# Performance work log

Hardware: AMD Instinct MI355X
Metric: run time of the kernel (lower is better)

The kernel has to match this reference:

```python
import jax, jax.numpy as jnp
import numpy as np

H = 16  # num_attention_heads


def setup_inputs() -> dict:
    key = jax.random.key(0)
    ks = jax.random.split(key, 4)
    B, S, D = 2, 2048, 1024
    hidden_states = jax.random.normal(ks[0], (B, S, D), dtype=jnp.float32)
    attention_mask = jnp.zeros((B, 1, 1, S), dtype=jnp.float32)
    scale = 1.0 / np.sqrt(D)
    Wq = jax.random.normal(ks[1], (D, D), dtype=jnp.float32) * scale
    Wk = jax.random.normal(ks[2], (D, D), dtype=jnp.float32) * scale
    Wv = jax.random.normal(ks[3], (D, D), dtype=jnp.float32) * scale
    bq = jnp.zeros((D,), dtype=jnp.float32)
    bk = jnp.zeros((D,), dtype=jnp.float32)
    bv = jnp.zeros((D,), dtype=jnp.float32)
    return {"hidden_states": hidden_states, "attention_mask": attention_mask,
            "Wq": Wq, "bq": bq, "Wk": Wk, "bk": bk, "Wv": Wv, "bv": bv}


def reference(hidden_states, attention_mask, Wq, bq, Wk, bk, Wv, bv):
    B, S, D = hidden_states.shape
    Dh = D // H

    def proj(W, b):
        # torch Linear: x @ W.T + b ; reshape to [B, H, S, Dh]
        y = jnp.einsum('bsd,ed->bse', hidden_states, W) + b
        return y.reshape(B, S, H, Dh).transpose(0, 2, 1, 3)

    q = proj(Wq, bq)
    k = proj(Wk, bk)
    v = proj(Wv, bv)

    scores = jnp.einsum('bhqd,bhkd->bhqk', q, k) / jnp.sqrt(jnp.float32(Dh))
    scores = scores + attention_mask  # additive mask broadcast [B,1,1,S]
    probs = jax.nn.softmax(scores, axis=-1)  # [B,H,Sq,Sk]
    out_attention_scores = probs.sum(axis=-2).sum(axis=-2)  # [B, Sk]
    # dropout prob = 0 (eval) -> identity
    context = jnp.einsum('bhqk,bhkd->bhqd', probs, v)
    context = context.transpose(0, 2, 1, 3).reshape(B, S, D)
    return context, out_attention_scores
```

## Files before the change

kernel.cpp:

```cpp
#include <hip/hip_runtime.h>
#include <hip/hip_bf16.h>
#include <stdint.h>

typedef unsigned short u16;
typedef __attribute__((ext_vector_type(8))) unsigned short u16x8;
typedef __attribute__((ext_vector_type(4))) unsigned short u16x4;
typedef __attribute__((ext_vector_type(8))) __bf16 bf16x8;
typedef __attribute__((ext_vector_type(4))) float f32x4;

#define LOG2E 1.44269504088896340736f

#if defined(__has_builtin)
#if __has_builtin(__builtin_amdgcn_exp2f)
#define EXP2(x) __builtin_amdgcn_exp2f(x)
#endif
#endif
#ifndef EXP2
#define EXP2(x) exp2f(x)
#endif

__device__ __forceinline__ f32x4 mfma16(u16x8 a, u16x8 b, f32x4 c) {
  return __builtin_amdgcn_mfma_f32_16x16x32_bf16(
      __builtin_bit_cast(bf16x8, a), __builtin_bit_cast(bf16x8, b), c, 0, 0, 0);
}

__device__ __forceinline__ u16 f2bf(float f) {
  unsigned u = __builtin_bit_cast(unsigned, f);
  return (u16)((u + 0x7fffu + ((u >> 16) & 1u)) >> 16);
}

__device__ __forceinline__ unsigned cvtpk(float a, float b) {
  unsigned r;
  asm volatile("v_cvt_pk_bf16_f32 %0, %1, %2" : "=v"(r) : "v"(a), "v"(b));
  return r;
}

__device__ __forceinline__ void gload_lds16(const void* g, void* l) {
  __builtin_amdgcn_global_load_lds(
      (__attribute__((address_space(1))) void*)const_cast<void*>(g),
      (__attribute__((address_space(3))) void*)l, 16, 0, 0);
}

template<int N> __device__ __forceinline__ void vmwait() {
  asm volatile("s_waitcnt vmcnt(%0)" :: "n"(N) : "memory");
  __builtin_amdgcn_sched_barrier(0);
}

#define SWZ(row, colbyte) ((((row) * 128) + (colbyte)) ^ (((row) & 7) << 4))

__global__ void cast_f32_bf16(const float* __restrict__ src, u16* __restrict__ dst, int n4) {
  int i = blockIdx.x * blockDim.x + threadIdx.x;
  if (i < n4) {
    f32x4 v = ((const f32x4*)src)[i];
    u16x4 o;
    o[0] = f2bf(v[0]); o[1] = f2bf(v[1]); o[2] = f2bf(v[2]); o[3] = f2bf(v[3]);
    ((u16x4*)dst)[i] = o;
  }
}

__global__ void cast3_f32_bf16(const float* __restrict__ s0, const float* __restrict__ s1,
                               const float* __restrict__ s2, u16* __restrict__ dst) {
  const int seg = blockIdx.x >> 10;
  const int i = (blockIdx.x & 1023) * blockDim.x + threadIdx.x;
  const float* src = (seg == 0) ? s0 : ((seg == 1) ? s1 : s2);
  f32x4 v = ((const f32x4*)src)[i];
  u16x4 o;
  o[0] = f2bf(v[0]); o[1] = f2bf(v[1]); o[2] = f2bf(v[2]); o[3] = f2bf(v[3]);
  ((u16x4*)(dst + (size_t)seg * 1048576))[i] = o;
}

__global__ __launch_bounds__(256) void gemm_qkv(
    const u16* __restrict__ A, const u16* __restrict__ Bm,
    const float* __restrict__ bq, const float* __restrict__ bk, const float* __restrict__ bv,
    u16* __restrict__ Qb, u16* __restrict__ Kb, u16* __restrict__ VTb) {
  __shared__ __align__(16) u16 Asm[3][4096];
  __shared__ __align__(16) u16 Bsm[3][4096];
  const int tid = threadIdx.x;
  const int wave = tid >> 6, lane = tid & 63;
  const int lq = lane & 15, lg = lane >> 4;
  const int wr = wave >> 1, wc = wave & 1;
  const int lin = blockIdx.y * 24 + blockIdx.x;
  const int wg = (lin & 7) * 96 + (lin >> 3);
  const int m0 = (wg / 24) * 128, n0 = (wg % 24) * 128;

  f32x4 zero = {0.f, 0.f, 0.f, 0.f};
  f32x4 acc[4][4];
#pragma unroll
  for (int mi = 0; mi < 4; ++mi)
#pragma unroll
    for (int ni = 0; ni < 4; ++ni) acc[mi][ni] = zero;

  auto stage = [&](int kt, int buf) {
    const int k0 = kt * 32;
#pragma unroll
    for (int c = 0; c < 2; ++c) {
      const int idx = wave * 2 + c;
      const u16* ga = A + (size_t)(m0 + idx * 16 + (lane >> 2)) * 1024 + k0 + (lane & 3) * 8;
      gload_lds16(ga, (char*)&Asm[buf][0] + idx * 1024);
      const u16* gb = Bm + (size_t)(n0 + idx * 16 + (lane >> 2)) * 1024 + k0 + (lane & 3) * 8;
      gload_lds16(gb, (char*)&Bsm[buf][0] + idx * 1024);
    }
  };

  stage(0, 0);
  stage(1, 1);
  for (int kt = 0; kt < 32; ++kt) {
    if (kt < 31) vmwait<4>(); else vmwait<0>();
    __builtin_amdgcn_s_barrier();
    if (kt + 2 < 32) stage(kt + 2, (kt + 2) % 3);
    const int cur = kt % 3;

    __builtin_amdgcn_s_setprio(1);
    u16x8 af[4], bfr[4];
#pragma unroll
    for (int mi = 0; mi < 4; ++mi)
      af[mi] = *(const u16x8*)&Asm[cur][(wr * 64 + mi * 16 + lq) * 32 + lg * 8];
#pragma unroll
    for (int ni = 0; ni < 4; ++ni)
      bfr[ni] = *(const u16x8*)&Bsm[cur][(wc * 64 + ni * 16 + lq) * 32 + lg * 8];
#pragma unroll
    for (int mi = 0; mi < 4; ++mi)
#pragma unroll
      for (int ni = 0; ni < 4; ++ni)
        acc[mi][ni] = mfma16(af[mi], bfr[ni], acc[mi][ni]);
    __builtin_amdgcn_s_setprio(0);
  }

  const int which = n0 >> 10;
  const float* bias = (which == 0) ? bq : ((which == 1) ? bk : bv);
  const float scl = (which == 0) ? (0.125f * LOG2E) : 1.0f;
#pragma unroll
  for (int mi = 0; mi < 4; ++mi) {
    const int m = m0 + wr * 64 + mi * 16 + lg * 4;
    const int bb = m >> 11;
    const int s = m & 2047;
#pragma unroll
    for (int ni = 0; ni < 4; ++ni) {
      const int n = n0 + wc * 64 + ni * 16 + lq;
      const int d = n & 1023;
      const int h = d >> 6, dh = d & 63;
      const float bi = bias[d];
#pragma unroll
      for (int r = 0; r < 4; ++r) {
        float v = (acc[mi][ni][r] + bi) * scl;
        if (which == 2)
          VTb[(((size_t)bb * 16 + h) * 64 + dh) * 2048 + (size_t)(s + r)] = f2bf(v);
        else {
          u16* dst = (which == 0) ? Qb : Kb;
          dst[(((size_t)bb * 16 + h) * 2048 + (size_t)(s + r)) * 64 + dh] = f2bf(v);
        }
      }
    }
  }
}

__global__ __launch_bounds__(512) void attn_main(
    const u16* __restrict__ Qb, const u16* __restrict__ Kb, const u16* __restrict__ VTb,
    const float* __restrict__ maskg, float* __restrict__ out_ctx, float* __restrict__ winv) {
  __shared__ __align__(16) u16 Kl[3][4096];
  __shared__ __align__(16) u16 VTl[3][4096];
  __shared__ __align__(16) u16 Pl[8][1024];

  const int tid = threadIdx.x;
  const int w = tid >> 6, lane = tid & 63;
  const int lq = lane & 15, lg = lane >> 4;
  const int bid = (blockIdx.x & 7) * 64 + (blockIdx.x >> 3);
  const int qt = bid & 15, bh = bid >> 4;
  const int b = bh >> 4, h = bh & 15;
  const int qw = qt * 128 + w * 16;

  const u16* qp = Qb + ((size_t)bh * 2048 + qw + lq) * 64 + lg * 8;
  const u16x8 qa0 = *(const u16x8*)qp;
  const u16x8 qa1 = *(const u16x8*)(qp + 32);

  const char* Kbase = (const char*)(Kb + (size_t)bh * 2048 * 64);
  const char* VTbase = (const char*)(VTb + (size_t)bh * 64 * 2048);
  const float* mbase = maskg + b * 2048;

  const int srow = tid >> 3;
  const int scol = ((tid & 7) * 16) ^ ((srow & 7) << 4);

  auto stageK = [&](int kt, int buf) {
    gload_lds16(Kbase + (size_t)(kt * 64 + srow) * 128 + scol, (char*)&Kl[buf][0] + w * 1024);
  };
  auto stageVT = [&](int kt, int buf) {
    gload_lds16(VTbase + (size_t)srow * 4096 + (size_t)kt * 128 + scol, (char*)&VTl[buf][0] + w * 1024);
  };

  f32x4 acc[4];
  {
    f32x4 zero = {0.f, 0.f, 0.f, 0.f};
#pragma unroll
    for (int ni = 0; ni < 4; ++ni) acc[ni] = zero;
  }
  float l_l = 0.f;
  char* Pw = (char*)&Pl[w][0];

  stageK(0, 0); stageVT(0, 0);
  stageK(1, 1); stageVT(1, 1);
  for (int kt = 0; kt < 32; ++kt) {
    if (kt < 31) vmwait<2>(); else vmwait<0>();
    __builtin_amdgcn_s_barrier();
    if (kt + 2 < 32) {
      const int nb = (kt + 2) % 3;
      stageK(kt + 2, nb);
      stageVT(kt + 2, nb);
    }
    const int cur = kt % 3;
    const char* Kt = (const char*)&Kl[cur][0];
    const char* Vt = (const char*)&VTl[cur][0];

    __builtin_amdgcn_s_setprio(1);
#pragma unroll
    for (int chunk = 0; chunk < 4; ++chunk) {
      const int krow = chunk * 16 + lq;
      const u16x8 ka0 = *(const u16x8*)(Kt + SWZ(krow, lg * 16));
      const u16x8 ka1 = *(const u16x8*)(Kt + SWZ(krow, 64 + lg * 16));
      f32x4 z = {0.f, 0.f, 0.f, 0.f};
      f32x4 s = mfma16(ka0, qa0, z);
      s = mfma16(ka1, qa1, s);
      const f32x4 mv = *(const f32x4*)(mbase + kt * 64 + chunk * 16 + lg * 4);
      float p[4];
#pragma unroll
      for (int r = 0; r < 4; ++r) {
        p[r] = EXP2(fmaf(mv[r], LOG2E, s[r]));
        l_l += p[r];
      }
      uint2 wp;
      wp.x = cvtpk(p[0], p[1]); wp.y = cvtpk(p[2], p[3]);
      *(uint2*)(Pw + SWZ(lq, chunk * 32 + lg * 8)) = wp;
    }

#pragma unroll
    for (int kc = 0; kc < 2; ++kc) {
      const u16x8 pa = *(const u16x8*)(Pw + SWZ(lq, kc * 64 + lg * 16));
#pragma unroll
      for (int ni = 0; ni < 4; ++ni) {
        const u16x8 vb = *(const u16x8*)(Vt + SWZ(ni * 16 + lq, kc * 64 + lg * 16));
        acc[ni] = mfma16(pa, vb, acc[ni]);
      }
    }
    __builtin_amdgcn_s_setprio(0);
  }

  l_l += __shfl_xor(l_l, 16);
  l_l += __shfl_xor(l_l, 32);
  const float il = 1.0f / l_l;
  if (lg == 0) winv[bh * 2048 + qw + lq] = il;

  f32x4 il4;
#pragma unroll
  for (int r = 0; r < 4; ++r) il4[r] = __shfl(il, lg * 4 + r);

  const int qrow = b * 2048 + qw + lg * 4;
#pragma unroll
  for (int ni = 0; ni < 4; ++ni) {
    const int dh = h * 64 + ni * 16 + lq;
#pragma unroll
    for (int r = 0; r < 4; ++r)
      out_ctx[(size_t)(qrow + r) * 1024 + dh] = acc[ni][r] * il4[r];
  }
}

__global__ __launch_bounds__(256) void colsum_kernel(
    const u16* __restrict__ Qb, const u16* __restrict__ Kb,
    const float* __restrict__ maskg, const float* __restrict__ winv,
    float* __restrict__ out_cs) {
  __shared__ __align__(16) u16 Ql[3][4096];

  const int tid = threadIdx.x;
  const int w = tid >> 6, lane = tid & 63;
  const int lq = lane & 15, lg = lane >> 4;
  const int bid = (blockIdx.x & 7) * 64 + (blockIdx.x >> 3);
  const int ktile = bid & 15, bh = bid >> 4;
  const int b = bh >> 4;
  const int kbase = ktile * 128 + w * 32;

  const u16* kp0 = Kb + ((size_t)bh * 2048 + kbase + lq) * 64 + lg * 8;
  const u16* kp1 = kp0 + 16 * 64;
  const u16x8 kb00 = *(const u16x8*)kp0, kb01 = *(const u16x8*)(kp0 + 32);
  const u16x8 kb10 = *(const u16x8*)kp1, kb11 = *(const u16x8*)(kp1 + 32);
  const float mvl0 = maskg[b * 2048 + kbase + lq] * LOG2E;
  const float mvl1 = maskg[b * 2048 + kbase + 16 + lq] * LOG2E;
  const float* wbase = winv + bh * 2048;
  const char* Qbase = (const char*)(Qb + (size_t)bh * 2048 * 64);

  const int r0 = tid >> 3;
  const int scol = ((tid & 7) * 16) ^ ((r0 & 7) << 4);
  auto stageQ = [&](int qt, int buf) {
    const char* src = Qbase + (size_t)(qt * 64) * 128;
    char* d = (char*)&Ql[buf][0] + w * 1024;
    gload_lds16(src + (size_t)r0 * 128 + scol, d);
    gload_lds16(src + (size_t)(r0 + 32) * 128 + scol, d + 4096);
  };

  float c0 = 0.f, c1 = 0.f;
  stageQ(0, 0);
  stageQ(1, 1);
  for (int qt = 0; qt < 32; ++qt) {
    if (qt < 31) vmwait<2>(); else vmwait<0>();
    __builtin_amdgcn_s_barrier();
    if (qt + 2 < 32) stageQ(qt + 2, (qt + 2) % 3);
    const char* Qt = (const char*)&Ql[qt % 3][0];
#pragma unroll
    for (int chunk = 0; chunk < 4; ++chunk) {
      const u16x8 qf0 = *(const u16x8*)(Qt + SWZ(chunk * 16 + lq, lg * 16));
      const u16x8 qf1 = *(const u16x8*)(Qt + SWZ(chunk * 16 + lq, 64 + lg * 16));
      f32x4 z = {0.f, 0.f, 0.f, 0.f};
      f32x4 s0 = mfma16(qf0, kb00, z);
      s0 = mfma16(qf1, kb01, s0);
      f32x4 s1 = mfma16(qf0, kb10, z);
      s1 = mfma16(qf1, kb11, s1);
      const f32x4 wv = *(const f32x4*)(wbase + qt * 64 + chunk * 16 + lg * 4);
#pragma unroll
      for (int r = 0; r < 4; ++r) {
        c0 += EXP2(s0[r] + mvl0) * wv[r];
        c1 += EXP2(s1[r] + mvl1) * wv[r];
      }
    }
  }
  c0 += __shfl_xor(c0, 16); c0 += __shfl_xor(c0, 32);
  c1 += __shfl_xor(c1, 16); c1 += __shfl_xor(c1, 32);
  if (lg == 0) {
    atomicAdd(&out_cs[b * 2048 + kbase + lq], c0);
    atomicAdd(&out_cs[b * 2048 + kbase + 16 + lq], c1);
  }
}

extern "C" void kernel_launch(void* const* d_in, const int* in_sizes, int n_in,
                              void* d_out, int out_size, void* d_ws, size_t ws_size,
                              hipStream_t stream) {
  (void)in_sizes; (void)n_in; (void)out_size; (void)ws_size;
  const float* X    = (const float*)d_in[0];
  const float* mask = (const float*)d_in[1];
  const float* Wq   = (const float*)d_in[2];
  const float* bq   = (const float*)d_in[3];
  const float* Wk   = (const float*)d_in[4];
  const float* bk   = (const float*)d_in[5];
  const float* Wv   = (const float*)d_in[6];
  const float* bv   = (const float*)d_in[7];
  float* out = (float*)d_out;

  char* ws = (char*)d_ws;
  u16* Xb   = (u16*)(ws);
  u16* Wcat = (u16*)(ws + 8388608);
  u16* Qb   = (u16*)(ws + 14680064);
  u16* Kb   = (u16*)(ws + 23068672);
  u16* VTb  = (u16*)(ws + 31457280);
  float* winv = (float*)(ws + 39845888);

  cast_f32_bf16<<<4096, 256, 0, stream>>>(X, Xb, 1048576);
  cast3_f32_bf16<<<3072, 256, 0, stream>>>(Wq, Wk, Wv, Wcat);

  hipMemsetAsync(out + 4194304, 0, 4096 * sizeof(float), stream);

  gemm_qkv<<<dim3(24, 32), 256, 0, stream>>>(Xb, Wcat, bq, bk, bv, Qb, Kb, VTb);

  attn_main<<<512, 512, 0, stream>>>(Qb, Kb, VTb, mask, out, winv);
  colsum_kernel<<<512, 256, 0, stream>>>(Qb, Kb, mask, winv, out + 4194304);
}
```

Before: 142.1 us.

## Switch attention to 32x32 MFMA with register-resident P via permlane swap

The attention kernel moves from 16x16x32 MFMA to 32x32x16 MFMA. Each wave now owns 32 query rows, so each block covers 256 queries and the grid halves to 256 blocks. The softmax probabilities are packed to bf16 and rearranged in registers with v_permlane32_swap rather than going through per-wave LDS buffers. That removes the LDS write/read round trip and raises MFMA work per fragment load. Prefetch staging is moved after compute in both attention and colsum kernels, with setprio around the compute. The trade-offs are fewer blocks on the GPU, which may lower occupancy or leave CUs under-filled, and more accumulator registers per wave.

```diff
diff --git a/kernel.cpp b/kernel.cpp
--- a/kernel.cpp
+++ b/kernel.cpp
@@ -7,6 +7,7 @@
 typedef __attribute__((ext_vector_type(4))) unsigned short u16x4;
 typedef __attribute__((ext_vector_type(8))) __bf16 bf16x8;
 typedef __attribute__((ext_vector_type(4))) float f32x4;
+typedef __attribute__((ext_vector_type(16))) float f32x16;
 
 #define LOG2E 1.44269504088896340736f
 
@@ -24,6 +25,11 @@
       __builtin_bit_cast(bf16x8, a), __builtin_bit_cast(bf16x8, b), c, 0, 0, 0);
 }
 
+__device__ __forceinline__ f32x16 mfma32(u16x8 a, u16x8 b, f32x16 c) {
+  return __builtin_amdgcn_mfma_f32_32x32x16_bf16(
+      __builtin_bit_cast(bf16x8, a), __builtin_bit_cast(bf16x8, b), c, 0, 0, 0);
+}
+
 __device__ __forceinline__ u16 f2bf(float f) {
   unsigned u = __builtin_bit_cast(unsigned, f);
   return (u16)((u + 0x7fffu + ((u >> 16) & 1u)) >> 16);
@@ -33,6 +39,10 @@
   unsigned r;
   asm volatile("v_cvt_pk_bf16_f32 %0, %1, %2" : "=v"(r) : "v"(a), "v"(b));
   return r;
+}
+
+__device__ __forceinline__ void pswap(unsigned& a, unsigned& b) {
+  asm volatile("v_permlane32_swap_b32 %0, %1" : "+v"(a), "+v"(b));
 }
 
 __device__ __forceinline__ void gload_lds16(const void* g, void* l) {
@@ -159,19 +169,20 @@
     const float* __restrict__ maskg, float* __restrict__ out_ctx, float* __restrict__ winv) {
   __shared__ __align__(16) u16 Kl[3][4096];
   __shared__ __align__(16) u16 VTl[3][4096];
-  __shared__ __align__(16) u16 Pl[8][1024];
+  __shared__ float sml[256];
 
   const int tid = threadIdx.x;
   const int w = tid >> 6, lane = tid & 63;
-  const int lq = lane & 15, lg = lane >> 4;
-  const int bid = (blockIdx.x & 7) * 64 + (blockIdx.x >> 3);
-  const int qt = bid & 15, bh = bid >> 4;
-  const int b = bh >> 4, h = bh & 15;
-  const int qw = qt * 128 + w * 16;
-
-  const u16* qp = Qb + ((size_t)bh * 2048 + qw + lq) * 64 + lg * 8;
-  const u16x8 qa0 = *(const u16x8*)qp;
-  const u16x8 qa1 = *(const u16x8*)(qp + 32);
+  const int l31 = lane & 31, h = lane >> 5;
+  const int bid = (blockIdx.x & 7) * 32 + (blockIdx.x >> 3);
+  const int qt = bid & 7, bh = bid >> 3;
+  const int b = bh >> 4, hh = bh & 15;
+  const int qw = qt * 256 + w * 32;
+
+  const u16* qp = Qb + ((size_t)bh * 2048 + qw + l31) * 64 + h * 8;
+  u16x8 qa[4];
+#pragma unroll
+  for (int dq = 0; dq < 4; ++dq) qa[dq] = *(const u16x8*)(qp + dq * 16);
 
   const char* Kbase = (const char*)(Kb + (size_t)bh * 2048 * 64);
   const char* VTbase = (const char*)(VTb + (size_t)bh * 64 * 2048);
@@ -179,7 +190,6 @@
 
   const int srow = tid >> 3;
   const int scol = ((tid & 7) * 16) ^ ((srow & 7) << 4);
-
   auto stageK = [&](int kt, int buf) {
     gload_lds16(Kbase + (size_t)(kt * 64 + srow) * 128 + scol, (char*)&Kl[buf][0] + w * 1024);
   };
@@ -187,78 +197,87 @@
     gload_lds16(VTbase + (size_t)srow * 4096 + (size_t)kt * 128 + scol, (char*)&VTl[buf][0] + w * 1024);
   };
 
-  f32x4 acc[4];
-  {
-    f32x4 zero = {0.f, 0.f, 0.f, 0.f};
-#pragma unroll
-    for (int ni = 0; ni < 4; ++ni) acc[ni] = zero;
-  }
+  f32x16 accpv[2];
+#pragma unroll
+  for (int db = 0; db < 2; ++db)
+#pragma unroll
+    for (int r = 0; r < 16; ++r) accpv[db][r] = 0.f;
   float l_l = 0.f;
-  char* Pw = (char*)&Pl[w][0];
 
   stageK(0, 0); stageVT(0, 0);
   stageK(1, 1); stageVT(1, 1);
   for (int kt = 0; kt < 32; ++kt) {
     if (kt < 31) vmwait<2>(); else vmwait<0>();
     __builtin_amdgcn_s_barrier();
+    const char* Kt = (const char*)&Kl[kt % 3][0];
+    const char* Vt = (const char*)&VTl[kt % 3][0];
+
+    __builtin_amdgcn_s_setprio(1);
+#pragma unroll
+    for (int kb = 0; kb < 2; ++kb) {
+      f32x16 s;
+#pragma unroll
+      for (int r = 0; r < 16; ++r) s[r] = 0.f;
+#pragma unroll
+      for (int dq = 0; dq < 4; ++dq) {
+        const u16x8 ka = *(const u16x8*)(Kt + SWZ(kb * 32 + l31, dq * 32 + h * 16));
+        s = mfma32(ka, qa[dq], s);
+      }
+      float p[16];
+#pragma unroll
+      for (int g = 0; g < 4; ++g) {
+        const f32x4 mv = *(const f32x4*)(mbase + kt * 64 + kb * 32 + g * 8 + h * 4);
+#pragma unroll
+        for (int j = 0; j < 4; ++j)
+          p[g * 4 + j] = EXP2(fmaf(mv[j], LOG2E, s[g * 4 + j]));
+      }
+      l_l += ((p[0] + p[1]) + (p[2] + p[3])) + ((p[4] + p[5]) + (p[6] + p[7])) +
+             ((p[8] + p[9]) + (p[10] + p[11])) + ((p[12] + p[13]) + (p[14] + p[15]));
+      unsigned a01 = cvtpk(p[0], p[1]), a23 = cvtpk(p[2], p[3]);
+      unsigned a45 = cvtpk(p[4], p[5]), a67 = cvtpk(p[6], p[7]);
+      unsigned b01 = cvtpk(p[8], p[9]), b23 = cvtpk(p[10], p[11]);
+      unsigned b45 = cvtpk(p[12], p[13]), b67 = cvtpk(p[14], p[15]);
+      pswap(a01, a45); pswap(a23, a67);
+      pswap(b01, b45); pswap(b23, b67);
+      uint4 f1 = {a01, a23, a45, a67};
+      uint4 f2 = {b01, b23, b45, b67};
+      u16x8 pf[2] = {__builtin_bit_cast(u16x8, f1), __builtin_bit_cast(u16x8, f2)};
+#pragma unroll
+      for (int ks2 = 0; ks2 < 2; ++ks2) {
+#pragma unroll
+        for (int db = 0; db < 2; ++db) {
+          const u16x8 vt = *(const u16x8*)(Vt + SWZ(db * 32 + l31, kb * 64 + ks2 * 32 + h * 16));
+          accpv[db] = mfma32(pf[ks2], vt, accpv[db]);
+        }
+      }
+    }
+    __builtin_amdgcn_s_setprio(0);
+    __builtin_amdgcn_sched_barrier(0);
     if (kt + 2 < 32) {
-      const int nb = (kt + 2) % 3;
-      stageK(kt + 2, nb);
-      stageVT(kt + 2, nb);
-    }
-    const int cur = kt % 3;
-    const char* Kt = (const char*)&Kl[cur][0];
-    const char* Vt = (const char*)&VTl[cur][0];
-
-    __builtin_amdgcn_s_setprio(1);
-#pragma unroll
-    for (int chunk = 0; chunk < 4; ++chunk) {
-      const int krow = chunk * 16 + lq;
-      const u16x8 ka0 = *(const u16x8*)(Kt + SWZ(krow, lg * 16));
-      const u16x8 ka1 = *(const u16x8*)(Kt + SWZ(krow, 64 + lg * 16));
-      f32x4 z = {0.f, 0.f, 0.f, 0.f};
-      f32x4 s = mfma16(ka0, qa0, z);
-      s = mfma16(ka1, qa1, s);
-      const f32x4 mv = *(const f32x4*)(mbase + kt * 64 + chunk * 16 + lg * 4);
-      float p[4];
-#pragma unroll
-      for (int r = 0; r < 4; ++r) {
-        p[r] = EXP2(fmaf(mv[r], LOG2E, s[r]));
-        l_l += p[r];
-      }
-      uint2 wp;
-      wp.x = cvtpk(p[0], p[1]); wp.y = cvtpk(p[2], p[3]);
-      *(uint2*)(Pw + SWZ(lq, chunk * 32 + lg * 8)) = wp;
-    }
-
-#pragma unroll
-    for (int kc = 0; kc < 2; ++kc) {
-      const u16x8 pa = *(const u16x8*)(Pw + SWZ(lq, kc * 64 + lg * 16));
-#pragma unroll
-      for (int ni = 0; ni < 4; ++ni) {
-        const u16x8 vb = *(const u16x8*)(Vt + SWZ(ni * 16 + lq, kc * 64 + lg * 16));
-        acc[ni] = mfma16(pa, vb, acc[ni]);
-      }
-    }
-    __builtin_amdgcn_s_setprio(0);
-  }
-
-  l_l += __shfl_xor(l_l, 16);
+      stageK(kt + 2, (kt + 2) % 3);
+      stageVT(kt + 2, (kt + 2) % 3);
+    }
+  }
+
   l_l += __shfl_xor(l_l, 32);
   const float il = 1.0f / l_l;
-  if (lg == 0) winv[bh * 2048 + qw + lq] = il;
-
-  f32x4 il4;
-#pragma unroll
-  for (int r = 0; r < 4; ++r) il4[r] = __shfl(il, lg * 4 + r);
-
-  const int qrow = b * 2048 + qw + lg * 4;
-#pragma unroll
-  for (int ni = 0; ni < 4; ++ni) {
-    const int dh = h * 64 + ni * 16 + lq;
-#pragma unroll
-    for (int r = 0; r < 4; ++r)
-      out_ctx[(size_t)(qrow + r) * 1024 + dh] = acc[ni][r] * il4[r];
+  if (h == 0) {
+    winv[bh * 2048 + qw + l31] = il;
+    sml[w * 32 + l31] = il;
+  }
+  __syncthreads();
+  f32x4 il4[4];
+#pragma unroll
+  for (int g = 0; g < 4; ++g) il4[g] = *(const f32x4*)&sml[w * 32 + g * 8 + h * 4];
+
+#pragma unroll
+  for (int db = 0; db < 2; ++db) {
+#pragma unroll
+    for (int r = 0; r < 16; ++r) {
+      const int q = qw + (r & 3) + (r >> 2) * 8 + h * 4;
+      out_ctx[(size_t)(b * 2048 + q) * 1024 + hh * 64 + db * 32 + l31] =
+          accpv[db][r] * il4[r >> 2][r & 3];
+    }
   }
 }
 
@@ -300,8 +319,8 @@
   for (int qt = 0; qt < 32; ++qt) {
     if (qt < 31) vmwait<2>(); else vmwait<0>();
     __builtin_amdgcn_s_barrier();
-    if (qt + 2 < 32) stageQ(qt + 2, (qt + 2) % 3);
     const char* Qt = (const char*)&Ql[qt % 3][0];
+    __builtin_amdgcn_s_setprio(1);
 #pragma unroll
     for (int chunk = 0; chunk < 4; ++chunk) {
       const u16x8 qf0 = *(const u16x8*)(Qt + SWZ(chunk * 16 + lq, lg * 16));
@@ -318,6 +337,9 @@
         c1 += EXP2(s1[r] + mvl1) * wv[r];
       }
     }
+    __builtin_amdgcn_s_setprio(0);
+    __builtin_amdgcn_sched_barrier(0);
+    if (qt + 2 < 32) stageQ(qt + 2, (qt + 2) % 3);
   }
   c0 += __shfl_xor(c0, 16); c0 += __shfl_xor(c0, 32);
   c1 += __shfl_xor(c1, 16); c1 += __shfl_xor(c1, 32);
@@ -356,6 +378,6 @@
 
   gemm_qkv<<<dim3(24, 32), 256, 0, stream>>>(Xb, Wcat, bq, bk, bv, Qb, Kb, VTb);
 
-  attn_main<<<512, 512, 0, stream>>>(Qb, Kb, VTb, mask, out, winv);
+  attn_main<<<256, 512, 0, stream>>>(Qb, Kb, VTb, mask, out, winv);
   colsum_kernel<<<512, 256, 0, stream>>>(Qb, Kb, mask, winv, out + 4194304);
 }
```

New measurement: 155.7 us. 9.5% more time.
